# Performance work log

Hardware: AMD Instinct MI355X
Metric: run time of the kernel (lower is better)

The kernel has to match this reference:

```python
import jax, jax.numpy as jnp
import numpy as np

B, T, C, H = 256, 256, 384, 64  # batch, seq (= block_size), n_embd, head_size


def setup_inputs() -> dict:
    key = jax.random.key(0)
    kx, kq, kk, kv = jax.random.split(key, 4)
    x = jax.random.normal(kx, (B, T, C), dtype=jnp.float32)
    # nn.Linear(n_embd, head_size, bias=False) weights, stored transposed so y = x @ W
    scale = 1.0 / np.sqrt(C)
    Wq = jax.random.normal(kq, (C, H), dtype=jnp.float32) * scale
    Wk = jax.random.normal(kk, (C, H), dtype=jnp.float32) * scale
    Wv = jax.random.normal(kv, (C, H), dtype=jnp.float32) * scale
    return {"x": x, "Wq": Wq, "Wk": Wk, "Wv": Wv}


def reference(x, Wq, Wk, Wv):
    # Single causal self-attention head. NOTE: source scales by C**-0.5 where
    # C = n_embd (not head_size) — preserved faithfully. Dropout in eval mode
    # (identity) for a deterministic reference.
    Bv, Tv, Cv = x.shape
    q = x @ Wq                                   # [B, T, H]
    k = x @ Wk                                   # [B, T, H]
    v = x @ Wv                                   # [B, T, H]
    wei = jnp.einsum('bth,bsh->bts', q, k) * (Cv ** -0.5)  # [B, T, T]
    causal = jnp.tril(jnp.ones((Tv, Tv), dtype=bool))      # tril[:T,:T]
    wei = jnp.where(causal[None, :, :], wei, -jnp.inf)
    wei = jax.nn.softmax(wei, axis=-1)
    out = jnp.einsum('bts,bsh->bth', wei, v)     # [B, T, H]
    return out
```

## Files before the change

### kernel.cpp

```cpp
#include <hip/hip_runtime.h>
#include <hip/hip_bf16.h>

typedef __attribute__((ext_vector_type(8))) short bf16x8;
typedef __attribute__((ext_vector_type(4))) float f32x4;

__device__ __forceinline__ unsigned short f2bf(float f) {
    union { float f; unsigned int u; } v; v.f = f;
    unsigned int u = v.u;
    unsigned int r = u + 0x7FFFu + ((u >> 16) & 1u);
    return (unsigned short)(r >> 16);
}

__device__ __forceinline__ unsigned int cvtpk(float lo, float hi) {
    unsigned int r;
    asm("v_cvt_pk_bf16_f32 %0, %1, %2" : "=v"(r) : "v"(lo), "v"(hi));
    return r;
}

#define GLDS16(gsrc, ldst)                                                          \
    __builtin_amdgcn_global_load_lds(                                               \
        (const __attribute__((address_space(1))) unsigned int*)(gsrc),              \
        (__attribute__((address_space(3))) unsigned int*)(ldst), 16, 0, 0)

__global__ __launch_bounds__(256) void wprep(const float* __restrict__ Wq,
                                             const float* __restrict__ Wk,
                                             const float* __restrict__ Wv,
                                             unsigned short* __restrict__ Wt2) {
    int idx = blockIdx.x * 256 + threadIdx.x;
    if (idx >= 73728) return;
    int w   = idx / 24576;
    int rem = idx % 24576;
    int n = rem / 384, k = rem % 384;
    const float* W = (w == 0) ? Wq : ((w == 1) ? Wk : Wv);
    int col = w * 64 + n;
    Wt2[(size_t)(k >> 5) * 6144 + ((k >> 3) & 3) * 1536 + col * 8 + (k & 7)] = f2bf(W[k * 64 + n]);
}

#define QOFF  0
#define KOFF  36864
#define VTOFF 73728
#define POFF  107520

template<int NT>
__device__ __forceinline__ void attn_strip(char* smem, char* Pw, float* ob,
                                           int r0, int l15, int lg) {
    const float scale = 0.05103103630798287f;

    bf16x8 aq[2][2];
#pragma unroll
    for (int m = 0; m < 2; ++m)
#pragma unroll
        for (int kk = 0; kk < 2; ++kk)
            aq[m][kk] = *reinterpret_cast<const bf16x8*>(smem + QOFF + ((r0 + m * 16 + l15) * 72 + kk * 32 + lg * 8) * 2);

    f32x4 s[NT][2][4] = {};
#pragma unroll
    for (int jt = 0; jt < NT; ++jt) {
#pragma unroll
        for (int kk = 0; kk < 2; ++kk) {
            bf16x8 bk[4];
#pragma unroll
            for (int n = 0; n < 4; ++n)
                bk[n] = *reinterpret_cast<const bf16x8*>(smem + KOFF + ((jt * 64 + n * 16 + l15) * 72 + kk * 32 + lg * 8) * 2);
#pragma unroll
            for (int m = 0; m < 2; ++m)
#pragma unroll
                for (int n = 0; n < 4; ++n)
                    s[jt][m][n] = __builtin_amdgcn_mfma_f32_16x16x32_bf16(aq[m][kk], bk[n], s[jt][m][n], 0, 0, 0);
        }
    }
    float M[2][4];
#pragma unroll
    for (int m = 0; m < 2; ++m)
#pragma unroll
        for (int j = 0; j < 4; ++j) M[m][j] = -1e30f;
#pragma unroll
    for (int jt = 0; jt < NT; ++jt)
#pragma unroll
        for (int m = 0; m < 2; ++m)
#pragma unroll
            for (int n = 0; n < 4; ++n) {
                int colg = jt * 64 + n * 16 + l15;
#pragma unroll
                for (int j = 0; j < 4; ++j) {
                    int rowg = r0 + m * 16 + lg * 4 + j;
                    float v = s[jt][m][n][j] * scale;
                    if (colg > rowg) v = -1e30f;
                    s[jt][m][n][j] = v;
                    M[m][j] = fmaxf(M[m][j], v);
                }
            }
#pragma unroll
    for (int m = 0; m < 2; ++m)
#pragma unroll
        for (int j = 0; j < 4; ++j) {
            float v = M[m][j];
            v = fmaxf(v, __shfl_xor(v, 1));
            v = fmaxf(v, __shfl_xor(v, 2));
            v = fmaxf(v, __shfl_xor(v, 4));
            v = fmaxf(v, __shfl_xor(v, 8));
            M[m][j] = v;
        }
    float L[2][4] = {};
#pragma unroll
    for (int jt = 0; jt < NT; ++jt)
#pragma unroll
        for (int m = 0; m < 2; ++m)
#pragma unroll
            for (int n = 0; n < 4; ++n)
#pragma unroll
                for (int j = 0; j < 4; ++j) {
                    float p = __expf(s[jt][m][n][j] - M[m][j]);
                    s[jt][m][n][j] = p;
                    L[m][j] += p;
                }
#pragma unroll
    for (int m = 0; m < 2; ++m)
#pragma unroll
        for (int j = 0; j < 4; ++j) {
            float v = L[m][j];
            v += __shfl_xor(v, 1);
            v += __shfl_xor(v, 2);
            v += __shfl_xor(v, 4);
            v += __shfl_xor(v, 8);
            L[m][j] = v;
        }
    f32x4 o[2][4] = {};
#pragma unroll
    for (int jt = 0; jt < NT; ++jt) {
#pragma unroll
        for (int m = 0; m < 2; ++m)
#pragma unroll
            for (int n = 0; n < 4; ++n)
#pragma unroll
                for (int j = 0; j < 4; ++j)
                    *reinterpret_cast<unsigned short*>(Pw + ((m * 16 + lg * 4 + j) * 72 + n * 16 + l15) * 2) = f2bf(s[jt][m][n][j]);
        asm volatile("s_waitcnt lgkmcnt(0)" ::: "memory");
#pragma unroll
        for (int kk = 0; kk < 2; ++kk) {
            bf16x8 ap[2], bv[4];
#pragma unroll
            for (int m = 0; m < 2; ++m)
                ap[m] = *reinterpret_cast<const bf16x8*>(Pw + ((m * 16 + l15) * 72 + kk * 32 + lg * 8) * 2);
#pragma unroll
            for (int n = 0; n < 4; ++n)
                bv[n] = *reinterpret_cast<const bf16x8*>(smem + VTOFF + ((n * 16 + l15) * 264 + jt * 64 + kk * 32 + lg * 8) * 2);
#pragma unroll
            for (int m = 0; m < 2; ++m)
#pragma unroll
                for (int n = 0; n < 4; ++n)
                    o[m][n] = __builtin_amdgcn_mfma_f32_16x16x32_bf16(ap[m], bv[n], o[m][n], 0, 0, 0);
        }
    }
#pragma unroll
    for (int m = 0; m < 2; ++m)
#pragma unroll
        for (int n = 0; n < 4; ++n) {
            int h = n * 16 + l15;
#pragma unroll
            for (int j = 0; j < 4; ++j) {
                int t = r0 + m * 16 + lg * 4 + j;
                ob[(size_t)t * 64 + h] = o[m][n][j] / L[m][j];
            }
        }
}

__global__ __launch_bounds__(512, 1) void fused(const float* __restrict__ x,
                                                const unsigned short* __restrict__ Wt2,
                                                float* __restrict__ out) {
    __shared__ __align__(16) char smem[147456];

    const int b = blockIdx.x;
    const int tid = threadIdx.x, lane = tid & 63, wid = tid >> 6;
    const int l15 = lane & 15, lg = lane >> 4;
    const float* xb = x + (size_t)b * 98304;
    float* ob = out + (size_t)b * 16384;

#pragma unroll
    for (int i = 0; i < 18; ++i) {
        int n = wid * 18 + i;
        GLDS16(Wt2 + (size_t)n * 512 + lane * 8, smem + n * 1024);
    }

    const float* xw = xb + (size_t)(wid * 32 + l15) * 384 + lg * 8;

    float4 p0[4], p1[4], p2[4], p3[4], p4[4];
#define XLOAD(P, C)                                                                 \
    P[0] = *reinterpret_cast<const float4*>(xw + (C) * 32);                         \
    P[1] = *reinterpret_cast<const float4*>(xw + (C) * 32 + 4);                     \
    P[2] = *reinterpret_cast<const float4*>(xw + 6144 + (C) * 32);                  \
    P[3] = *reinterpret_cast<const float4*>(xw + 6144 + (C) * 32 + 4);
    XLOAD(p0, 0)
    XLOAD(p1, 1)
    XLOAD(p2, 2)
    XLOAD(p3, 3)
    XLOAD(p4, 4)
    __builtin_amdgcn_sched_barrier(0);
    asm volatile("s_waitcnt vmcnt(20)" ::: "memory");
    __builtin_amdgcn_s_barrier();

    f32x4 acc[2][12] = {};

#define CHUNK(C, P, WAITN)                                                          \
    asm volatile("s_waitcnt vmcnt(" #WAITN ")" ::: "memory");                       \
    __builtin_amdgcn_sched_barrier(0);                                              \
    {                                                                               \
        union { unsigned int u[4]; bf16x8 v; } cv0, cv1;                            \
        cv0.u[0] = cvtpk(P[0].x, P[0].y); cv0.u[1] = cvtpk(P[0].z, P[0].w);         \
        cv0.u[2] = cvtpk(P[1].x, P[1].y); cv0.u[3] = cvtpk(P[1].z, P[1].w);         \
        cv1.u[0] = cvtpk(P[2].x, P[2].y); cv1.u[1] = cvtpk(P[2].z, P[2].w);         \
        cv1.u[2] = cvtpk(P[3].x, P[3].y); cv1.u[3] = cvtpk(P[3].z, P[3].w);         \
        bf16x8 a0 = cv0.v, a1 = cv1.v;                                              \
        if ((C) + 5 < 12) { XLOAD(P, (C) + 5) }                                     \
        __builtin_amdgcn_sched_barrier(0);                                          \
        const char* bs = smem + (C) * 12288 + lg * 3072 + l15 * 16;                 \
        _Pragma("unroll")                                                           \
        for (int n = 0; n < 12; ++n) {                                              \
            bf16x8 bf = *reinterpret_cast<const bf16x8*>(bs + n * 256);             \
            acc[0][n] = __builtin_amdgcn_mfma_f32_16x16x32_bf16(a0, bf, acc[0][n], 0, 0, 0); \
            acc[1][n] = __builtin_amdgcn_mfma_f32_16x16x32_bf16(a1, bf, acc[1][n], 0, 0, 0); \
        }                                                                           \
    }

    CHUNK(0,  p0, 16)
    CHUNK(1,  p1, 16)
    CHUNK(2,  p2, 16)
    CHUNK(3,  p3, 16)
    CHUNK(4,  p4, 16)
    CHUNK(5,  p0, 16)
    CHUNK(6,  p1, 16)
    CHUNK(7,  p2, 16)
    CHUNK(8,  p3, 12)
    CHUNK(9,  p4, 8)
    CHUNK(10, p0, 4)
    CHUNK(11, p1, 0)

    __syncthreads();

#pragma unroll
    for (int m = 0; m < 2; ++m) {
#pragma unroll
        for (int n = 0; n < 12; ++n) {
            int col = n * 16 + l15;
#pragma unroll
            for (int j = 0; j < 4; ++j) {
                int t = wid * 32 + m * 16 + lg * 4 + j;
                unsigned short hv = f2bf(acc[m][n][j]);
                if (col < 64)
                    *reinterpret_cast<unsigned short*>(smem + QOFF + (t * 72 + col) * 2) = hv;
                else if (col < 128)
                    *reinterpret_cast<unsigned short*>(smem + KOFF + (t * 72 + (col - 64)) * 2) = hv;
                else
                    *reinterpret_cast<unsigned short*>(smem + VTOFF + ((col - 128) * 264 + t) * 2) = hv;
            }
        }
    }
    __syncthreads();

    char* Pw = smem + POFF + wid * 4608;
    const int r0 = wid * 32;
    if (wid < 2)      attn_strip<1>(smem, Pw, ob, r0, l15, lg);
    else if (wid < 4) attn_strip<2>(smem, Pw, ob, r0, l15, lg);
    else if (wid < 6) attn_strip<3>(smem, Pw, ob, r0, l15, lg);
    else              attn_strip<4>(smem, Pw, ob, r0, l15, lg);
}

extern "C" void kernel_launch(void* const* d_in, const int* in_sizes, int n_in,
                              void* d_out, int out_size, void* d_ws, size_t ws_size,
                              hipStream_t stream) {
    const float* x  = (const float*)d_in[0];
    const float* Wq = (const float*)d_in[1];
    const float* Wk = (const float*)d_in[2];
    const float* Wv = (const float*)d_in[3];
    float* out = (float*)d_out;

    unsigned short* Wt2 = (unsigned short*)d_ws;

    wprep<<<288, 256, 0, stream>>>(Wq, Wk, Wv, Wt2);
    fused<<<256, 512, 0, stream>>>(x, Wt2, out);
}
```

Measured before the change: 39.49 us.

## Balance causal attention across waves with paired 16-row strips

Attention now runs as 16-row strips, and each wave handles a short strip paired with a long one (rows w and 15-w). Before, each wave owned one 32-row strip, so the causal work per wave varied fourfold. The causal mask is applied only on the diagonal tile, and normalisation uses a reciprocal instead of a divide. Outputs are staged through LDS so global stores are coalesced float4 writes, and V is written transposed as vectorized ushort4 stores. The costs are smaller MFMA reuse per Q load, one extra LDS round trip for the output, and an approximate rcp.

New measurement: 38.30 us. -3.0%, faster.

```diff
diff --git a/kernel.cpp b/kernel.cpp
--- a/kernel.cpp
+++ b/kernel.cpp
@@ -14,6 +14,12 @@
 __device__ __forceinline__ unsigned int cvtpk(float lo, float hi) {
     unsigned int r;
     asm("v_cvt_pk_bf16_f32 %0, %1, %2" : "=v"(r) : "v"(lo), "v"(hi));
+    return r;
+}
+
+__device__ __forceinline__ float frcp(float x) {
+    float r;
+    asm("v_rcp_f32 %0, %1" : "=v"(r) : "v"(x));
     return r;
 }
 
@@ -42,20 +48,19 @@
 #define POFF  107520
 
 template<int NT>
-__device__ __forceinline__ void attn_strip(char* smem, char* Pw, float* ob,
-                                           int r0, int l15, int lg) {
+__device__ __forceinline__ void attn_strip16(char* smem, char* Pw, float* __restrict__ ob,
+                                             int r0, int lane) {
+    const int l15 = lane & 15, lg = lane >> 4;
     const float scale = 0.05103103630798287f;
 
-    bf16x8 aq[2][2];
-#pragma unroll
-    for (int m = 0; m < 2; ++m)
-#pragma unroll
-        for (int kk = 0; kk < 2; ++kk)
-            aq[m][kk] = *reinterpret_cast<const bf16x8*>(smem + QOFF + ((r0 + m * 16 + l15) * 72 + kk * 32 + lg * 8) * 2);
-
-    f32x4 s[NT][2][4] = {};
-#pragma unroll
-    for (int jt = 0; jt < NT; ++jt) {
+    bf16x8 aq[2];
+#pragma unroll
+    for (int kk = 0; kk < 2; ++kk)
+        aq[kk] = *reinterpret_cast<const bf16x8*>(smem + QOFF + ((r0 + l15) * 72 + kk * 32 + lg * 8) * 2);
+
+    f32x4 s[NT][4] = {};
+#pragma unroll
+    for (int jt = 0; jt < NT; ++jt)
 #pragma unroll
         for (int kk = 0; kk < 2; ++kk) {
             bf16x8 bk[4];
@@ -63,106 +68,93 @@
             for (int n = 0; n < 4; ++n)
                 bk[n] = *reinterpret_cast<const bf16x8*>(smem + KOFF + ((jt * 64 + n * 16 + l15) * 72 + kk * 32 + lg * 8) * 2);
 #pragma unroll
-            for (int m = 0; m < 2; ++m)
-#pragma unroll
-                for (int n = 0; n < 4; ++n)
-                    s[jt][m][n] = __builtin_amdgcn_mfma_f32_16x16x32_bf16(aq[m][kk], bk[n], s[jt][m][n], 0, 0, 0);
-        }
-    }
-    float M[2][4];
-#pragma unroll
-    for (int m = 0; m < 2; ++m)
-#pragma unroll
-        for (int j = 0; j < 4; ++j) M[m][j] = -1e30f;
+            for (int n = 0; n < 4; ++n)
+                s[jt][n] = __builtin_amdgcn_mfma_f32_16x16x32_bf16(aq[kk], bk[n], s[jt][n], 0, 0, 0);
+        }
+
+    float M[4];
+#pragma unroll
+    for (int j = 0; j < 4; ++j) M[j] = -1e30f;
 #pragma unroll
     for (int jt = 0; jt < NT; ++jt)
 #pragma unroll
-        for (int m = 0; m < 2; ++m)
-#pragma unroll
-            for (int n = 0; n < 4; ++n) {
-                int colg = jt * 64 + n * 16 + l15;
-#pragma unroll
-                for (int j = 0; j < 4; ++j) {
-                    int rowg = r0 + m * 16 + lg * 4 + j;
-                    float v = s[jt][m][n][j] * scale;
+        for (int n = 0; n < 4; ++n) {
+            int colg = jt * 64 + n * 16 + l15;
+#pragma unroll
+            for (int j = 0; j < 4; ++j) {
+                float v = s[jt][n][j] * scale;
+                if (jt == NT - 1) {
+                    int rowg = r0 + lg * 4 + j;
                     if (colg > rowg) v = -1e30f;
-                    s[jt][m][n][j] = v;
-                    M[m][j] = fmaxf(M[m][j], v);
                 }
+                s[jt][n][j] = v;
+                M[j] = fmaxf(M[j], v);
             }
-#pragma unroll
-    for (int m = 0; m < 2; ++m)
-#pragma unroll
-        for (int j = 0; j < 4; ++j) {
-            float v = M[m][j];
-            v = fmaxf(v, __shfl_xor(v, 1));
-            v = fmaxf(v, __shfl_xor(v, 2));
-            v = fmaxf(v, __shfl_xor(v, 4));
-            v = fmaxf(v, __shfl_xor(v, 8));
-            M[m][j] = v;
-        }
-    float L[2][4] = {};
+        }
+#pragma unroll
+    for (int j = 0; j < 4; ++j) {
+        float v = M[j];
+        v = fmaxf(v, __shfl_xor(v, 1));
+        v = fmaxf(v, __shfl_xor(v, 2));
+        v = fmaxf(v, __shfl_xor(v, 4));
+        v = fmaxf(v, __shfl_xor(v, 8));
+        M[j] = v;
+    }
+    float L[4] = {};
 #pragma unroll
     for (int jt = 0; jt < NT; ++jt)
 #pragma unroll
-        for (int m = 0; m < 2; ++m)
-#pragma unroll
-            for (int n = 0; n < 4; ++n)
-#pragma unroll
-                for (int j = 0; j < 4; ++j) {
-                    float p = __expf(s[jt][m][n][j] - M[m][j]);
-                    s[jt][m][n][j] = p;
-                    L[m][j] += p;
-                }
-#pragma unroll
-    for (int m = 0; m < 2; ++m)
-#pragma unroll
-        for (int j = 0; j < 4; ++j) {
-            float v = L[m][j];
-            v += __shfl_xor(v, 1);
-            v += __shfl_xor(v, 2);
-            v += __shfl_xor(v, 4);
-            v += __shfl_xor(v, 8);
-            L[m][j] = v;
-        }
-    f32x4 o[2][4] = {};
+        for (int n = 0; n < 4; ++n)
+#pragma unroll
+            for (int j = 0; j < 4; ++j) {
+                float p = __expf(s[jt][n][j] - M[j]);
+                s[jt][n][j] = p;
+                L[j] += p;
+            }
+    float rL[4];
+#pragma unroll
+    for (int j = 0; j < 4; ++j) {
+        float v = L[j];
+        v += __shfl_xor(v, 1);
+        v += __shfl_xor(v, 2);
+        v += __shfl_xor(v, 4);
+        v += __shfl_xor(v, 8);
+        rL[j] = frcp(v);
+    }
+    f32x4 o[4] = {};
 #pragma unroll
     for (int jt = 0; jt < NT; ++jt) {
 #pragma unroll
-        for (int m = 0; m < 2; ++m)
-#pragma unroll
-            for (int n = 0; n < 4; ++n)
-#pragma unroll
-                for (int j = 0; j < 4; ++j)
-                    *reinterpret_cast<unsigned short*>(Pw + ((m * 16 + lg * 4 + j) * 72 + n * 16 + l15) * 2) = f2bf(s[jt][m][n][j]);
+        for (int n = 0; n < 4; ++n)
+#pragma unroll
+            for (int j = 0; j < 4; ++j)
+                *reinterpret_cast<unsigned short*>(Pw + ((lg * 4 + j) * 72 + n * 16 + l15) * 2) = f2bf(s[jt][n][j]);
         asm volatile("s_waitcnt lgkmcnt(0)" ::: "memory");
 #pragma unroll
         for (int kk = 0; kk < 2; ++kk) {
-            bf16x8 ap[2], bv[4];
-#pragma unroll
-            for (int m = 0; m < 2; ++m)
-                ap[m] = *reinterpret_cast<const bf16x8*>(Pw + ((m * 16 + l15) * 72 + kk * 32 + lg * 8) * 2);
+            bf16x8 ap, bv[4];
+            ap = *reinterpret_cast<const bf16x8*>(Pw + (l15 * 72 + kk * 32 + lg * 8) * 2);
 #pragma unroll
             for (int n = 0; n < 4; ++n)
                 bv[n] = *reinterpret_cast<const bf16x8*>(smem + VTOFF + ((n * 16 + l15) * 264 + jt * 64 + kk * 32 + lg * 8) * 2);
 #pragma unroll
-            for (int m = 0; m < 2; ++m)
-#pragma unroll
-                for (int n = 0; n < 4; ++n)
-                    o[m][n] = __builtin_amdgcn_mfma_f32_16x16x32_bf16(ap[m], bv[n], o[m][n], 0, 0, 0);
-        }
-    }
-#pragma unroll
-    for (int m = 0; m < 2; ++m)
-#pragma unroll
-        for (int n = 0; n < 4; ++n) {
-            int h = n * 16 + l15;
-#pragma unroll
-            for (int j = 0; j < 4; ++j) {
-                int t = r0 + m * 16 + lg * 4 + j;
-                ob[(size_t)t * 64 + h] = o[m][n][j] / L[m][j];
-            }
-        }
+            for (int n = 0; n < 4; ++n)
+                o[n] = __builtin_amdgcn_mfma_f32_16x16x32_bf16(ap, bv[n], o[n], 0, 0, 0);
+        }
+    }
+    float* tf = reinterpret_cast<float*>(Pw);
+#pragma unroll
+    for (int n = 0; n < 4; ++n)
+#pragma unroll
+        for (int j = 0; j < 4; ++j)
+            tf[(lg * 4 + j) * 68 + n * 16 + l15] = o[n][j] * rL[j];
+    asm volatile("s_waitcnt lgkmcnt(0)" ::: "memory");
+#pragma unroll
+    for (int i = 0; i < 4; ++i) {
+        int row = i * 4 + lg;
+        float4 vv = *reinterpret_cast<const float4*>(&tf[row * 68 + l15 * 4]);
+        *reinterpret_cast<float4*>(ob + (size_t)(r0 + row) * 64 + l15 * 4) = vv;
+    }
 }
 
 __global__ __launch_bounds__(512, 1) void fused(const float* __restrict__ x,
@@ -239,30 +231,40 @@
 
 #pragma unroll
     for (int m = 0; m < 2; ++m) {
-#pragma unroll
-        for (int n = 0; n < 12; ++n) {
+        const int t0 = wid * 32 + m * 16 + lg * 4;
+#pragma unroll
+        for (int n = 0; n < 4; ++n) {
             int col = n * 16 + l15;
 #pragma unroll
-            for (int j = 0; j < 4; ++j) {
-                int t = wid * 32 + m * 16 + lg * 4 + j;
-                unsigned short hv = f2bf(acc[m][n][j]);
-                if (col < 64)
-                    *reinterpret_cast<unsigned short*>(smem + QOFF + (t * 72 + col) * 2) = hv;
-                else if (col < 128)
-                    *reinterpret_cast<unsigned short*>(smem + KOFF + (t * 72 + (col - 64)) * 2) = hv;
-                else
-                    *reinterpret_cast<unsigned short*>(smem + VTOFF + ((col - 128) * 264 + t) * 2) = hv;
-            }
+            for (int j = 0; j < 4; ++j)
+                *reinterpret_cast<unsigned short*>(smem + QOFF + ((t0 + j) * 72 + col) * 2) = f2bf(acc[m][n][j]);
+        }
+#pragma unroll
+        for (int n = 4; n < 8; ++n) {
+            int col = (n - 4) * 16 + l15;
+#pragma unroll
+            for (int j = 0; j < 4; ++j)
+                *reinterpret_cast<unsigned short*>(smem + KOFF + ((t0 + j) * 72 + col) * 2) = f2bf(acc[m][n][j]);
+        }
+#pragma unroll
+        for (int n = 8; n < 12; ++n) {
+            int h = (n - 8) * 16 + l15;
+            ushort4 h4;
+            h4.x = f2bf(acc[m][n][0]); h4.y = f2bf(acc[m][n][1]);
+            h4.z = f2bf(acc[m][n][2]); h4.w = f2bf(acc[m][n][3]);
+            *reinterpret_cast<ushort4*>(smem + VTOFF + (h * 264 + t0) * 2) = h4;
         }
     }
     __syncthreads();
 
     char* Pw = smem + POFF + wid * 4608;
-    const int r0 = wid * 32;
-    if (wid < 2)      attn_strip<1>(smem, Pw, ob, r0, l15, lg);
-    else if (wid < 4) attn_strip<2>(smem, Pw, ob, r0, l15, lg);
-    else if (wid < 6) attn_strip<3>(smem, Pw, ob, r0, l15, lg);
-    else              attn_strip<4>(smem, Pw, ob, r0, l15, lg);
+    if (wid < 4) {
+        attn_strip16<1>(smem, Pw, ob, wid * 16, lane);
+        attn_strip16<4>(smem, Pw, ob, (15 - wid) * 16, lane);
+    } else {
+        attn_strip16<2>(smem, Pw, ob, wid * 16, lane);
+        attn_strip16<3>(smem, Pw, ob, (15 - wid) * 16, lane);
+    }
 }
 
 extern "C" void kernel_launch(void* const* d_in, const int* in_sizes, int n_in,
```
